# Kernel optimization log

Hardware: AMD Instinct MI355X
Metric: run time of the kernel (lower is better)

The kernel has to match this reference:

```python
import jax, jax.numpy as jnp
import numpy as np

N = 50000      # nodes
E = 800000     # edges
H = 64         # hid_dim (== in_dim)
T = 4          # number of S2V message-passing steps


def setup_inputs() -> dict:
    key = jax.random.key(0)
    ks = jax.random.split(key, 12)
    mu = jax.random.normal(ks[0], (N, H), dtype=jnp.float32)
    x = jax.random.uniform(ks[1], (N, 1), dtype=jnp.float32)
    edge_index = jax.random.randint(ks[2], (2, E), 0, N, dtype=jnp.int64)
    edge_w = jax.random.uniform(ks[3], (E, 1), dtype=jnp.float32)
    s = 0.05  # small init scale to keep activations bounded across T relu layers
    W1 = jax.random.normal(ks[4], (T, H, 1), dtype=jnp.float32) * s   # lin1 per layer, torch [out,in]
    W2 = jax.random.normal(ks[5], (T, H, H), dtype=jnp.float32) * s   # lin2 per layer
    W3 = jax.random.normal(ks[6], (T, H, H), dtype=jnp.float32) * s   # lin3 per layer
    W4 = jax.random.normal(ks[7], (T, H, 1), dtype=jnp.float32) * s   # lin4 per layer
    W5 = jax.random.normal(ks[8], (1, 2 * H), dtype=jnp.float32) * s  # lin5
    W7 = jax.random.normal(ks[9], (H, H), dtype=jnp.float32) * s      # lin7
    return {"mu": mu, "x": x, "edge_index": edge_index, "edge_w": edge_w,
            "W1": W1, "W2": W2, "W3": W3, "W4": W4, "W5": W5, "W7": W7}


def _s2v_step(mu, x, idx, edge_w, w1, w2, w3, w4):
    # Faithful to source: gather AND scatter both use edge_index[1].
    x_emb = x @ w1.T                                            # [N,H]
    mu_j = mu[idx]                                              # [E,H] gather
    mu_aggr = jax.ops.segment_sum(mu_j, idx, num_segments=N)    # [N,H] scatter_add
    mu_aggr = mu_aggr @ w2.T
    ew = jax.nn.relu(edge_w @ w4.T)                             # [E,H]
    ew_aggr = jax.ops.segment_sum(ew, idx, num_segments=N)      # [N,H]
    ew_aggr = ew_aggr @ w3.T
    return jax.nn.relu(x_emb + mu_aggr + ew_aggr)


def reference(mu, x, edge_index, edge_w, W1, W2, W3, W4, W5, W7):
    idx = edge_index[1]
    for t in range(T):
        mu = _s2v_step(mu, x, idx, edge_w, W1[t], W2[t], W3[t], W4[t])
    nodes_vec = mu @ W7.T                                       # [N,H]
    graph_pool = jnp.broadcast_to(jnp.sum(mu, axis=0, keepdims=True), (N, H))
    cat = jnp.concatenate([graph_pool, nodes_vec], axis=1)      # [N,2H]
    return (jax.nn.relu(cat) @ W5.T).squeeze(-1)                # [N]
```

## Files before the change

kernel.cpp:

```cpp
#include <hip/hip_runtime.h>

#define H 64
#define NPB 64
#define KS 104
#define KSD 52

typedef short bf16x8 __attribute__((ext_vector_type(8)));
typedef float f32x4 __attribute__((ext_vector_type(4)));

static __device__ __forceinline__ unsigned short f2bf(float f) {
    union { float f; unsigned u; } v; v.f = f;
    unsigned r = v.u + 0x7fffu + ((v.u >> 16) & 1u);
    return (unsigned short)(r >> 16);
}
static __device__ __forceinline__ float bf2f(unsigned short b) {
    union { unsigned u; float f; } v; v.u = ((unsigned)b) << 16;
    return v.f;
}
static __device__ __forceinline__ void split8(const float* ff, bf16x8& hi, bf16x8& lo) {
#pragma unroll
    for (int j = 0; j < 8; ++j) {
        unsigned short h = f2bf(ff[j]);
        hi[j] = (short)h;
        lo[j] = (short)f2bf(ff[j] - bf2f(h));
    }
}

__global__ void edge_kernel(const int* __restrict__ ei, const float* __restrict__ ew,
                            double* __restrict__ dS, int E) {
    int probe = ei[2 * (threadIdx.x & 63) + 1];
    bool is64 = (__ballot(probe != 0) == 0ULL);
    int e = blockIdx.x * blockDim.x + threadIdx.x;
    if (e >= E) return;
    int idx = is64 ? ei[2 * (E + e)] : ei[E + e];
    unsafeAtomicAdd(&dS[idx], 4096.0 + (double)ew[e]);
}

__global__ __launch_bounds__(256, 2)
void node_kernel(const float* __restrict__ mu, const float* __restrict__ x,
                 const float* __restrict__ W1, const float* __restrict__ W2,
                 const float* __restrict__ W3, const float* __restrict__ W4,
                 const float* __restrict__ W5, const float* __restrict__ W7,
                 const double* __restrict__ dS, float* __restrict__ gp,
                 float* __restrict__ out, int N) {
    __shared__ unsigned short Ab[2][NPB * KS];
    __shared__ float v3s[4 * H];
    __shared__ float degs[NPB];
    __shared__ float red[4 * NPB];

    const int t = threadIdx.x;
    const int lane = t & 63;
    const int w = __builtin_amdgcn_readfirstlane(t >> 6);
    const int c = lane & 15;
    const int q = lane >> 4;
    const int hh = 16 * w + c;
    const int base = blockIdx.x * NPB;

    {
        unsigned* a = (unsigned*)&Ab[0][0];
        for (int i = t; i < 2 * NPB * KSD; i += 256) a[i] = 0;
    }
    {
        const float* __restrict__ w3r = W3 + (w * H + lane) * H;
        const float* __restrict__ w4r = W4 + w * H;
        float a0 = 0, a1 = 0, a2 = 0, a3 = 0;
#pragma unroll
        for (int k = 0; k < H; k += 4) {
            a0 += fmaxf(w4r[k + 0], 0.f) * w3r[k + 0];
            a1 += fmaxf(w4r[k + 1], 0.f) * w3r[k + 1];
            a2 += fmaxf(w4r[k + 2], 0.f) * w3r[k + 2];
            a3 += fmaxf(w4r[k + 3], 0.f) * w3r[k + 3];
        }
        v3s[w * H + lane] = (a0 + a1) + (a2 + a3);
    }
    __syncthreads();

    if (t < 64) {
        int node = base + t;
        float dg = 0.f, sv = 0.f, xv = 0.f;
        if (node < N) {
            double T = dS[node];
            double k = floor(T * (1.0 / 4096.0));
            dg = (float)k;
            sv = (float)(T - 4096.0 * k);
            xv = x[node];
        }
        degs[t] = dg;
        unsigned short xb = f2bf(xv), sb = f2bf(sv);
        Ab[0][t * KS + 64] = xb; Ab[0][t * KS + 65] = sb;
        Ab[1][t * KS + 64] = xb; Ab[1][t * KS + 65] = sb;
    }
    __syncthreads();

    {
        const float* __restrict__ mublk = mu + (size_t)base * H;
        const int maxf = (N - base) * H;
#pragma unroll
        for (int cc = 0; cc < 4; ++cc) {
            int f = (t + 256 * cc) * 4;
            float4 v = make_float4(0.f, 0.f, 0.f, 0.f);
            if (f < maxf) v = *(const float4*)(mublk + f);
            int m = f >> 6, k = f & 63;
            float dg = degs[m];
            ushort4 b;
            b.x = f2bf(v.x * dg); b.y = f2bf(v.y * dg);
            b.z = f2bf(v.z * dg); b.w = f2bf(v.w * dg);
            *(ushort4*)(&Ab[0][m * KS + k]) = b;
        }
    }
    __syncthreads();

    unsigned short* Acur = &Ab[0][0];
    unsigned short* Anxt = &Ab[1][0];

    for (int tl = 0; tl < 4; ++tl) {
        bf16x8 bh[3], bl[3];
#pragma unroll
        for (int s = 0; s < 2; ++s) {
            const float* __restrict__ wp = W2 + (tl * H + hh) * H + s * 32 + q * 8;
            float4 f0 = *(const float4*)(wp);
            float4 f1 = *(const float4*)(wp + 4);
            float ff[8] = {f0.x, f0.y, f0.z, f0.w, f1.x, f1.y, f1.z, f1.w};
            split8(ff, bh[s], bl[s]);
        }
        {
            float ff[8] = {0, 0, 0, 0, 0, 0, 0, 0};
            if (q == 0) { ff[0] = W1[tl * H + hh]; ff[1] = v3s[tl * H + hh]; }
            split8(ff, bh[2], bl[2]);
        }

        f32x4 acc[4];
#pragma unroll
        for (int mt = 0; mt < 4; ++mt)
#pragma unroll
            for (int r = 0; r < 4; ++r) acc[mt][r] = 0.f;

#pragma unroll
        for (int mt = 0; mt < 4; ++mt) {
            const unsigned short* ar = Acur + (mt * 16 + c) * KS;
            bf16x8 a0 = *(const bf16x8*)(ar + q * 8);
            bf16x8 a1 = *(const bf16x8*)(ar + 32 + q * 8);
            bf16x8 a2 = *(const bf16x8*)(ar + 64 + q * 8);
            acc[mt] = __builtin_amdgcn_mfma_f32_16x16x32_bf16(a0, bh[0], acc[mt], 0, 0, 0);
            acc[mt] = __builtin_amdgcn_mfma_f32_16x16x32_bf16(a0, bl[0], acc[mt], 0, 0, 0);
            acc[mt] = __builtin_amdgcn_mfma_f32_16x16x32_bf16(a1, bh[1], acc[mt], 0, 0, 0);
            acc[mt] = __builtin_amdgcn_mfma_f32_16x16x32_bf16(a1, bl[1], acc[mt], 0, 0, 0);
            acc[mt] = __builtin_amdgcn_mfma_f32_16x16x32_bf16(a2, bh[2], acc[mt], 0, 0, 0);
            acc[mt] = __builtin_amdgcn_mfma_f32_16x16x32_bf16(a2, bl[2], acc[mt], 0, 0, 0);
        }

        const bool scale = (tl < 3);
#pragma unroll
        for (int mt = 0; mt < 4; ++mt) {
#pragma unroll
            for (int r = 0; r < 4; ++r) {
                int m = mt * 16 + q * 4 + r;
                float v = fmaxf(acc[mt][r], 0.f);
                if (scale) v *= degs[m];
                Anxt[m * KS + hh] = f2bf(v);
            }
        }
        __syncthreads();
        unsigned short* tmp = Acur; Acur = Anxt; Anxt = tmp;
    }

    {
        bf16x8 bh[2], bl[2];
#pragma unroll
        for (int s = 0; s < 2; ++s) {
            const float* __restrict__ wp = W7 + hh * H + s * 32 + q * 8;
            float4 f0 = *(const float4*)(wp);
            float4 f1 = *(const float4*)(wp + 4);
            float ff[8] = {f0.x, f0.y, f0.z, f0.w, f1.x, f1.y, f1.z, f1.w};
            split8(ff, bh[s], bl[s]);
        }
        f32x4 acc[4];
#pragma unroll
        for (int mt = 0; mt < 4; ++mt)
#pragma unroll
            for (int r = 0; r < 4; ++r) acc[mt][r] = 0.f;
#pragma unroll
        for (int mt = 0; mt < 4; ++mt) {
            const unsigned short* ar = Acur + (mt * 16 + c) * KS;
            bf16x8 a0 = *(const bf16x8*)(ar + q * 8);
            bf16x8 a1 = *(const bf16x8*)(ar + 32 + q * 8);
            acc[mt] = __builtin_amdgcn_mfma_f32_16x16x32_bf16(a0, bh[0], acc[mt], 0, 0, 0);
            acc[mt] = __builtin_amdgcn_mfma_f32_16x16x32_bf16(a0, bl[0], acc[mt], 0, 0, 0);
            acc[mt] = __builtin_amdgcn_mfma_f32_16x16x32_bf16(a1, bh[1], acc[mt], 0, 0, 0);
            acc[mt] = __builtin_amdgcn_mfma_f32_16x16x32_bf16(a1, bl[1], acc[mt], 0, 0, 0);
        }
        float w5v = W5[H + hh];
#pragma unroll
        for (int mt = 0; mt < 4; ++mt) {
#pragma unroll
            for (int r = 0; r < 4; ++r) {
                float v = fmaxf(acc[mt][r], 0.f) * w5v;
                v += __shfl_xor(v, 1);
                v += __shfl_xor(v, 2);
                v += __shfl_xor(v, 4);
                v += __shfl_xor(v, 8);
                if (c == 0) red[w * 64 + mt * 16 + q * 4 + r] = v;
            }
        }
    }
    __syncthreads();
    if (t < 64) {
        float pn = red[t] + red[64 + t] + red[128 + t] + red[192 + t];
        if (base + t < N) out[base + t] = pn;
    }
    __syncthreads();

    {
        int h = t & 63, mq = t >> 6;
        float s = 0.f;
#pragma unroll
        for (int i = 0; i < 16; ++i) s += bf2f(Acur[(mq * 16 + i) * KS + h]);
        red[t] = s;
    }
    __syncthreads();
    if (t < 64) {
        float g = red[t] + red[64 + t] + red[128 + t] + red[192 + t];
        unsafeAtomicAdd(&gp[t], g);
    }
}

__global__ void finalize_kernel(const float* __restrict__ gp, const float* __restrict__ W5,
                                float* __restrict__ out, int N) {
    int n = blockIdx.x * blockDim.x + threadIdx.x;
    float C = 0.f;
#pragma unroll
    for (int h = 0; h < H; ++h) C += fmaxf(gp[h], 0.f) * W5[h];
    if (n < N) out[n] += C;
}

extern "C" void kernel_launch(void* const* d_in, const int* in_sizes, int n_in,
                              void* d_out, int out_size, void* d_ws, size_t ws_size,
                              hipStream_t stream) {
    const float* mu = (const float*)d_in[0];
    const float* x  = (const float*)d_in[1];
    const int*   ei = (const int*)d_in[2];
    const float* ew = (const float*)d_in[3];
    const float* W1 = (const float*)d_in[4];
    const float* W2 = (const float*)d_in[5];
    const float* W3 = (const float*)d_in[6];
    const float* W4 = (const float*)d_in[7];
    const float* W5 = (const float*)d_in[8];
    const float* W7 = (const float*)d_in[9];
    float* out = (float*)d_out;

    const int N = in_sizes[1];
    const int E = in_sizes[3];

    double* dS = (double*)d_ws;
    float*  gp = (float*)((char*)d_ws + (size_t)N * 8);

    hipMemsetAsync(d_ws, 0, (size_t)N * 8 + 64 * 4, stream);

    edge_kernel<<<(E + 255) / 256, 256, 0, stream>>>(ei, ew, dS, E);
    node_kernel<<<(N + NPB - 1) / NPB, 256, 0, stream>>>(mu, x, W1, W2, W3, W4,
                                                         W5, W7, dS, gp, out, N);
    finalize_kernel<<<(N + 255) / 256, 256, 0, stream>>>(gp, W5, out, N);
}
```

Before: 154.7 us.

## Precompute split bf16 weights in prep kernel, vectorize edge atomics, fold memset

```diff
diff --git a/kernel.cpp b/kernel.cpp
--- a/kernel.cpp
+++ b/kernel.cpp
@@ -3,8 +3,6 @@
 #define H 64
 #define NPB 64
 #define KS 104
-#define KSD 52
-
 typedef short bf16x8 __attribute__((ext_vector_type(8)));
 typedef float f32x4 __attribute__((ext_vector_type(4)));
 
@@ -26,25 +24,105 @@
     }
 }
 
-__global__ void edge_kernel(const int* __restrict__ ei, const float* __restrict__ ew,
-                            double* __restrict__ dS, int E) {
+
+__global__ __launch_bounds__(256)
+void prep_kernel(const float* __restrict__ W1, const float* __restrict__ W2,
+                 const float* __restrict__ W3, const float* __restrict__ W4,
+                 const float* __restrict__ W7, unsigned* __restrict__ zero_base,
+                 int zero_dwords, bf16x8* __restrict__ Bp, bf16x8* __restrict__ W7p) {
+    const int t = threadIdx.x;
+    if (blockIdx.x != 0) {
+        int idx = (blockIdx.x - 1) * 256 + t;
+        for (int i = idx; i < zero_dwords; i += 64 * 256) zero_base[i] = 0u;
+        return;
+    }
+    __shared__ float v3s[4 * H];
+    {
+        int tl = t >> 6, h = t & 63;
+        const float* __restrict__ w3r = W3 + (tl * H + h) * H;
+        const float* __restrict__ w4r = W4 + tl * H;
+        float a0 = 0, a1 = 0, a2 = 0, a3 = 0;
+#pragma unroll
+        for (int k = 0; k < H; k += 4) {
+            a0 += fmaxf(w4r[k + 0], 0.f) * w3r[k + 0];
+            a1 += fmaxf(w4r[k + 1], 0.f) * w3r[k + 1];
+            a2 += fmaxf(w4r[k + 2], 0.f) * w3r[k + 2];
+            a3 += fmaxf(w4r[k + 3], 0.f) * w3r[k + 3];
+        }
+        v3s[t] = (a0 + a1) + (a2 + a3);
+    }
+    __syncthreads();
+    const int w = t >> 6, lane = t & 63, c = lane & 15, q = lane >> 4;
+    const int hh = 16 * w + c;
+    for (int tl = 0; tl < 4; ++tl) {
+        const int b3 = (tl * 4 + w) * 3;
+        bf16x8 hi, lo;
+#pragma unroll
+        for (int s = 0; s < 2; ++s) {
+            const float* __restrict__ wp = W2 + (tl * H + hh) * H + s * 32 + q * 8;
+            float4 f0 = *(const float4*)(wp);
+            float4 f1 = *(const float4*)(wp + 4);
+            float ff[8] = {f0.x, f0.y, f0.z, f0.w, f1.x, f1.y, f1.z, f1.w};
+            split8(ff, hi, lo);
+            Bp[(b3 + s) * 128 + lane] = hi;
+            Bp[(b3 + s) * 128 + 64 + lane] = lo;
+        }
+        float ff[8] = {0, 0, 0, 0, 0, 0, 0, 0};
+        if (q == 0) { ff[0] = W1[tl * H + hh]; ff[1] = v3s[tl * H + hh]; }
+        split8(ff, hi, lo);
+        Bp[(b3 + 2) * 128 + lane] = hi;
+        Bp[(b3 + 2) * 128 + 64 + lane] = lo;
+    }
+#pragma unroll
+    for (int s = 0; s < 2; ++s) {
+        const float* __restrict__ wp = W7 + hh * H + s * 32 + q * 8;
+        float4 f0 = *(const float4*)(wp);
+        float4 f1 = *(const float4*)(wp + 4);
+        float ff[8] = {f0.x, f0.y, f0.z, f0.w, f1.x, f1.y, f1.z, f1.w};
+        bf16x8 hi, lo;
+        split8(ff, hi, lo);
+        W7p[(w * 2 + s) * 128 + lane] = hi;
+        W7p[(w * 2 + s) * 128 + 64 + lane] = lo;
+    }
+}
+
+__global__ __launch_bounds__(256)
+void edge_kernel(const int* __restrict__ ei, const float* __restrict__ ew,
+                 double* __restrict__ dS, int E) {
     int probe = ei[2 * (threadIdx.x & 63) + 1];
     bool is64 = (__ballot(probe != 0) == 0ULL);
-    int e = blockIdx.x * blockDim.x + threadIdx.x;
-    if (e >= E) return;
-    int idx = is64 ? ei[2 * (E + e)] : ei[E + e];
-    unsafeAtomicAdd(&dS[idx], 4096.0 + (double)ew[e]);
+    int e0 = 4 * (blockIdx.x * blockDim.x + threadIdx.x);
+    if (e0 >= E) return;
+    if (e0 + 3 < E) {
+        float4 wv = *(const float4*)(ew + e0);
+        int i0, i1, i2, i3;
+        if (is64) {
+            int4 a = *(const int4*)(ei + 2 * (E + e0));
+            int4 b = *(const int4*)(ei + 2 * (E + e0) + 4);
+            i0 = a.x; i1 = a.z; i2 = b.x; i3 = b.z;
+        } else {
+            int4 a = *(const int4*)(ei + E + e0);
+            i0 = a.x; i1 = a.y; i2 = a.z; i3 = a.w;
+        }
+        unsafeAtomicAdd(&dS[i0], 4096.0 + (double)wv.x);
+        unsafeAtomicAdd(&dS[i1], 4096.0 + (double)wv.y);
+        unsafeAtomicAdd(&dS[i2], 4096.0 + (double)wv.z);
+        unsafeAtomicAdd(&dS[i3], 4096.0 + (double)wv.w);
+    } else {
+        for (int j = 0; j < 4 && e0 + j < E; ++j) {
+            int e = e0 + j;
+            int idx = is64 ? ei[2 * (E + e)] : ei[E + e];
+            unsafeAtomicAdd(&dS[idx], 4096.0 + (double)ew[e]);
+        }
+    }
 }
 
 __global__ __launch_bounds__(256, 2)
 void node_kernel(const float* __restrict__ mu, const float* __restrict__ x,
-                 const float* __restrict__ W1, const float* __restrict__ W2,
-                 const float* __restrict__ W3, const float* __restrict__ W4,
-                 const float* __restrict__ W5, const float* __restrict__ W7,
-                 const double* __restrict__ dS, float* __restrict__ gp,
-                 float* __restrict__ out, int N) {
+                 const float* __restrict__ W5, const bf16x8* __restrict__ Bp,
+                 const bf16x8* __restrict__ W7p, const double* __restrict__ dS,
+                 float* __restrict__ gp, float* __restrict__ out, int N) {
     __shared__ unsigned short Ab[2][NPB * KS];
-    __shared__ float v3s[4 * H];
     __shared__ float degs[NPB];
     __shared__ float red[4 * NPB];
 
@@ -56,25 +134,12 @@
     const int hh = 16 * w + c;
     const int base = blockIdx.x * NPB;
 
-    {
-        unsigned* a = (unsigned*)&Ab[0][0];
-        for (int i = t; i < 2 * NPB * KSD; i += 256) a[i] = 0;
-    }
-    {
-        const float* __restrict__ w3r = W3 + (w * H + lane) * H;
-        const float* __restrict__ w4r = W4 + w * H;
-        float a0 = 0, a1 = 0, a2 = 0, a3 = 0;
-#pragma unroll
-        for (int k = 0; k < H; k += 4) {
-            a0 += fmaxf(w4r[k + 0], 0.f) * w3r[k + 0];
-            a1 += fmaxf(w4r[k + 1], 0.f) * w3r[k + 1];
-            a2 += fmaxf(w4r[k + 2], 0.f) * w3r[k + 2];
-            a3 += fmaxf(w4r[k + 3], 0.f) * w3r[k + 3];
-        }
-        v3s[w * H + lane] = (a0 + a1) + (a2 + a3);
-    }
-    __syncthreads();
-
+    if (t < 128) {
+        int buf = t >> 6, row = t & 63;
+        unsigned* p = (unsigned*)&Ab[buf][row * KS];
+#pragma unroll
+        for (int d = 33; d < 52; ++d) p[d] = 0u;
+    }
     if (t < 64) {
         int node = base + t;
         float dg = 0.f, sv = 0.f, xv = 0.f;
@@ -114,20 +179,10 @@
     unsigned short* Anxt = &Ab[1][0];
 
     for (int tl = 0; tl < 4; ++tl) {
-        bf16x8 bh[3], bl[3];
-#pragma unroll
-        for (int s = 0; s < 2; ++s) {
-            const float* __restrict__ wp = W2 + (tl * H + hh) * H + s * 32 + q * 8;
-            float4 f0 = *(const float4*)(wp);
-            float4 f1 = *(const float4*)(wp + 4);
-            float ff[8] = {f0.x, f0.y, f0.z, f0.w, f1.x, f1.y, f1.z, f1.w};
-            split8(ff, bh[s], bl[s]);
-        }
-        {
-            float ff[8] = {0, 0, 0, 0, 0, 0, 0, 0};
-            if (q == 0) { ff[0] = W1[tl * H + hh]; ff[1] = v3s[tl * H + hh]; }
-            split8(ff, bh[2], bl[2]);
-        }
+        const int b3 = (tl * 4 + w) * 3;
+        bf16x8 bh0 = Bp[(b3 + 0) * 128 + lane], bl0 = Bp[(b3 + 0) * 128 + 64 + lane];
+        bf16x8 bh1 = Bp[(b3 + 1) * 128 + lane], bl1 = Bp[(b3 + 1) * 128 + 64 + lane];
+        bf16x8 bh2 = Bp[(b3 + 2) * 128 + lane], bl2 = Bp[(b3 + 2) * 128 + 64 + lane];
 
         f32x4 acc[4];
 #pragma unroll
@@ -141,12 +196,12 @@
             bf16x8 a0 = *(const bf16x8*)(ar + q * 8);
             bf16x8 a1 = *(const bf16x8*)(ar + 32 + q * 8);
             bf16x8 a2 = *(const bf16x8*)(ar + 64 + q * 8);
-            acc[mt] = __builtin_amdgcn_mfma_f32_16x16x32_bf16(a0, bh[0], acc[mt], 0, 0, 0);
-            acc[mt] = __builtin_amdgcn_mfma_f32_16x16x32_bf16(a0, bl[0], acc[mt], 0, 0, 0);
-            acc[mt] = __builtin_amdgcn_mfma_f32_16x16x32_bf16(a1, bh[1], acc[mt], 0, 0, 0);
-            acc[mt] = __builtin_amdgcn_mfma_f32_16x16x32_bf16(a1, bl[1], acc[mt], 0, 0, 0);
-            acc[mt] = __builtin_amdgcn_mfma_f32_16x16x32_bf16(a2, bh[2], acc[mt], 0, 0, 0);
-            acc[mt] = __builtin_amdgcn_mfma_f32_16x16x32_bf16(a2, bl[2], acc[mt], 0, 0, 0);
+            acc[mt] = __builtin_amdgcn_mfma_f32_16x16x32_bf16(a0, bh0, acc[mt], 0, 0, 0);
+            acc[mt] = __builtin_amdgcn_mfma_f32_16x16x32_bf16(a0, bl0, acc[mt], 0, 0, 0);
+            acc[mt] = __builtin_amdgcn_mfma_f32_16x16x32_bf16(a1, bh1, acc[mt], 0, 0, 0);
+            acc[mt] = __builtin_amdgcn_mfma_f32_16x16x32_bf16(a1, bl1, acc[mt], 0, 0, 0);
+            acc[mt] = __builtin_amdgcn_mfma_f32_16x16x32_bf16(a2, bh2, acc[mt], 0, 0, 0);
+            acc[mt] = __builtin_amdgcn_mfma_f32_16x16x32_bf16(a2, bl2, acc[mt], 0, 0, 0);
         }
 
         const bool scale = (tl < 3);
@@ -165,15 +220,8 @@
     }
 
     {
-        bf16x8 bh[2], bl[2];
-#pragma unroll
-        for (int s = 0; s < 2; ++s) {
-            const float* __restrict__ wp = W7 + hh * H + s * 32 + q * 8;
-            float4 f0 = *(const float4*)(wp);
-            float4 f1 = *(const float4*)(wp + 4);
-            float ff[8] = {f0.x, f0.y, f0.z, f0.w, f1.x, f1.y, f1.z, f1.w};
-            split8(ff, bh[s], bl[s]);
-        }
+        bf16x8 bh0 = W7p[(w * 2 + 0) * 128 + lane], bl0 = W7p[(w * 2 + 0) * 128 + 64 + lane];
+        bf16x8 bh1 = W7p[(w * 2 + 1) * 128 + lane], bl1 = W7p[(w * 2 + 1) * 128 + 64 + lane];
         f32x4 acc[4];
 #pragma unroll
         for (int mt = 0; mt < 4; ++mt)
@@ -184,10 +232,10 @@
             const unsigned short* ar = Acur + (mt * 16 + c) * KS;
             bf16x8 a0 = *(const bf16x8*)(ar + q * 8);
             bf16x8 a1 = *(const bf16x8*)(ar + 32 + q * 8);
-            acc[mt] = __builtin_amdgcn_mfma_f32_16x16x32_bf16(a0, bh[0], acc[mt], 0, 0, 0);
-            acc[mt] = __builtin_amdgcn_mfma_f32_16x16x32_bf16(a0, bl[0], acc[mt], 0, 0, 0);
-            acc[mt] = __builtin_amdgcn_mfma_f32_16x16x32_bf16(a1, bh[1], acc[mt], 0, 0, 0);
-            acc[mt] = __builtin_amdgcn_mfma_f32_16x16x32_bf16(a1, bl[1], acc[mt], 0, 0, 0);
+            acc[mt] = __builtin_amdgcn_mfma_f32_16x16x32_bf16(a0, bh0, acc[mt], 0, 0, 0);
+            acc[mt] = __builtin_amdgcn_mfma_f32_16x16x32_bf16(a0, bl0, acc[mt], 0, 0, 0);
+            acc[mt] = __builtin_amdgcn_mfma_f32_16x16x32_bf16(a1, bh1, acc[mt], 0, 0, 0);
+            acc[mt] = __builtin_amdgcn_mfma_f32_16x16x32_bf16(a1, bl1, acc[mt], 0, 0, 0);
         }
         float w5v = W5[H + hh];
 #pragma unroll
@@ -224,13 +272,19 @@
     }
 }
 
-__global__ void finalize_kernel(const float* __restrict__ gp, const float* __restrict__ W5,
-                                float* __restrict__ out, int N) {
+__global__ __launch_bounds__(256)
+void finalize_kernel(const float* __restrict__ gp, const float* __restrict__ W5,
+                     float* __restrict__ out, int N) {
+    int lane = threadIdx.x & 63;
+    float v = fmaxf(gp[lane], 0.f) * W5[lane];
+    v += __shfl_xor(v, 1);
+    v += __shfl_xor(v, 2);
+    v += __shfl_xor(v, 4);
+    v += __shfl_xor(v, 8);
+    v += __shfl_xor(v, 16);
+    v += __shfl_xor(v, 32);
     int n = blockIdx.x * blockDim.x + threadIdx.x;
-    float C = 0.f;
-#pragma unroll
-    for (int h = 0; h < H; ++h) C += fmaxf(gp[h], 0.f) * W5[h];
-    if (n < N) out[n] += C;
+    if (n < N) out[n] += v;
 }
 
 extern "C" void kernel_launch(void* const* d_in, const int* in_sizes, int n_in,
@@ -251,13 +305,17 @@
     const int N = in_sizes[1];
     const int E = in_sizes[3];
 
-    double* dS = (double*)d_ws;
-    float*  gp = (float*)((char*)d_ws + (size_t)N * 8);
-
-    hipMemsetAsync(d_ws, 0, (size_t)N * 8 + 64 * 4, stream);
-
-    edge_kernel<<<(E + 255) / 256, 256, 0, stream>>>(ei, ew, dS, E);
-    node_kernel<<<(N + NPB - 1) / NPB, 256, 0, stream>>>(mu, x, W1, W2, W3, W4,
-                                                         W5, W7, dS, gp, out, N);
+    char* ws = (char*)d_ws;
+    double* dS  = (double*)ws;
+    float*  gp  = (float*)(ws + (size_t)N * 8);
+    bf16x8* Bp  = (bf16x8*)(ws + (size_t)N * 8 + 256);
+    bf16x8* W7p = (bf16x8*)(ws + (size_t)N * 8 + 256 + 196608);
+    int zero_dwords = N * 2 + 64;
+
+    prep_kernel<<<65, 256, 0, stream>>>(W1, W2, W3, W4, W7, (unsigned*)dS,
+                                        zero_dwords, Bp, W7p);
+    edge_kernel<<<(E + 1023) / 1024, 256, 0, stream>>>(ei, ew, dS, E);
+    node_kernel<<<(N + NPB - 1) / NPB, 256, 0, stream>>>(mu, x, W5, Bp, W7p,
+                                                         dS, gp, out, N);
     finalize_kernel<<<(N + 255) / 256, 256, 0, stream>>>(gp, W5, out, N);
 }
```

After: 150.2 us. -2.9%, faster.
